# Optimization experiments

Hardware: AMD Instinct MI355X
Metric: run time of the kernel (lower is better)

Reference implementation:

```python
import math
import jax, jax.numpy as jnp
import numpy as np

B, N, D, H, NI, NL, NS, MID = 32, 2048, 256, 8, 64, 3, 32, 3


def _ln(x, g, b, eps=1e-5):
    m = jnp.mean(x, axis=-1, keepdims=True)
    v = jnp.mean((x - m) ** 2, axis=-1, keepdims=True)
    return (x - m) * jax.lax.rsqrt(v + eps) * g + b


def _mab(Q, K, mask, Wq, bq, Wk, bk, Wv, bv, Wo, bo, g0, b0, g1, b1):
    # torch's split(dim_split,2)+cat(...,0) == reshape to (B, n, H, dh)
    dh = D // H
    q = (Q @ Wq + bq).reshape(Q.shape[0], Q.shape[1], H, dh)
    k = (K @ Wk + bk).reshape(K.shape[0], K.shape[1], H, dh)
    v = (K @ Wv + bv).reshape(K.shape[0], K.shape[1], H, dh)
    A = jnp.einsum('bqhd,bkhd->bhqk', q, k) / math.sqrt(D)  # note: sqrt(dim_V), faithful
    A = jnp.where(mask[:, None, None, :] == 0, -1e4, A)
    A = jax.nn.softmax(A, axis=-1)
    o = q + jnp.einsum('bhqk,bkhd->bqhd', A, v)
    O = o.reshape(Q.shape[0], Q.shape[1], D)
    O = _ln(O, g0, b0)
    O = O + jax.nn.relu(O @ Wo + bo)
    return _ln(O, g1, b1)


def _forward(x_values, y_target, point_mask, proj_W, proj_b, isab_I,
             isab_Wq, isab_bq, isab_Wk, isab_bk, isab_Wv, isab_bv,
             isab_Wo, isab_bo, isab_g0, isab_b0, isab_g1, isab_b1,
             pma_S, pma_Wq, pma_bq, pma_Wk, pma_bk, pma_Wv, pma_bv,
             pma_Wo, pma_bo, pma_g0, pma_b0, pma_g1, pma_b1):
    # input_dim == max_input_dim, so the zero-padded feature build is a concat
    feats = jnp.concatenate([x_values, y_target[..., None]], axis=-1)  # (B, N, MID+1)
    x = jax.nn.gelu(feats @ proj_W + proj_b, approximate=False)
    ones_mask = jnp.ones((x.shape[0], NI), jnp.float32)
    stk = (isab_Wq, isab_bq, isab_Wk, isab_bk, isab_Wv, isab_bv,
           isab_Wo, isab_bo, isab_g0, isab_b0, isab_g1, isab_b1)
    for l in range(NL):
        I = jnp.broadcast_to(isab_I[l][None], (x.shape[0], NI, D))
        h = _mab(I, x, point_mask, *[a[l, 0] for a in stk])   # mab0: inducing pts attend to X
        x = _mab(x, h, ones_mask, *[a[l, 1] for a in stk])    # mab1: X attends to H (all valid)
    S = jnp.broadcast_to(pma_S[None], (x.shape[0], NS, D))
    return _mab(S, x, point_mask, pma_Wq, pma_bq, pma_Wk, pma_bk, pma_Wv,
                pma_bv, pma_Wo, pma_bo, pma_g0, pma_b0, pma_g1, pma_b1)


def setup_inputs():
    key = jax.random.key(0)
    ks = iter(jax.random.split(key, 40))
    def nrm(shape, s=0.05):
        return jax.random.normal(next(ks), shape, dtype=jnp.float32) * s
    z = lambda shape: jnp.zeros(shape, jnp.float32)
    o = lambda shape: jnp.ones(shape, jnp.float32)
    return {
        'x_values': jax.random.normal(next(ks), (B, N, MID), jnp.float32),
        'y_target': jax.random.normal(next(ks), (B, N), jnp.float32),
        'point_mask': jax.random.randint(next(ks), (B, N), 0, 2).astype(jnp.float32),
        'proj_W': nrm((MID + 1, D)), 'proj_b': z((D,)),
        'isab_I': nrm((NL, NI, D), 0.1),
        'isab_Wq': nrm((NL, 2, D, D)), 'isab_bq': z((NL, 2, D)),
        'isab_Wk': nrm((NL, 2, D, D)), 'isab_bk': z((NL, 2, D)),
        'isab_Wv': nrm((NL, 2, D, D)), 'isab_bv': z((NL, 2, D)),
        'isab_Wo': nrm((NL, 2, D, D)), 'isab_bo': z((NL, 2, D)),
        'isab_g0': o((NL, 2, D)), 'isab_b0': z((NL, 2, D)),
        'isab_g1': o((NL, 2, D)), 'isab_b1': z((NL, 2, D)),
        'pma_S': nrm((NS, D), 0.1),
        'pma_Wq': nrm((D, D)), 'pma_bq': z((D,)),
        'pma_Wk': nrm((D, D)), 'pma_bk': z((D,)),
        'pma_Wv': nrm((D, D)), 'pma_bv': z((D,)),
        'pma_Wo': nrm((D, D)), 'pma_bo': z((D,)),
        'pma_g0': o((D,)), 'pma_b0': z((D,)),
        'pma_g1': o((D,)), 'pma_b1': z((D,)),
    }


def reference(x_values, y_target, point_mask, proj_W, proj_b, isab_I,
              isab_Wq, isab_bq, isab_Wk, isab_bk, isab_Wv, isab_bv,
              isab_Wo, isab_bo, isab_g0, isab_b0, isab_g1, isab_b1,
              pma_S, pma_Wq, pma_bq, pma_Wk, pma_bk, pma_Wv, pma_bv,
              pma_Wo, pma_bo, pma_g0, pma_b0, pma_g1, pma_b1):
    return _forward(x_values, y_target, point_mask, proj_W, proj_b, isab_I,
                    isab_Wq, isab_bq, isab_Wk, isab_bk, isab_Wv, isab_bv,
                    isab_Wo, isab_bo, isab_g0, isab_b0, isab_g1, isab_b1,
                    pma_S, pma_Wq, pma_bq, pma_Wk, pma_bk, pma_Wv, pma_bv,
                    pma_Wo, pma_bo, pma_g0, pma_b0, pma_g1, pma_b1)
```

## Files before the change

### kernel.cpp

```cpp
#include <hip/hip_runtime.h>
#include <hip/hip_bf16.h>


typedef __attribute__((ext_vector_type(8))) short short8;
typedef __attribute__((ext_vector_type(4))) float f32x4;
typedef __attribute__((ext_vector_type(4))) ushort ushort4v;

__device__ __forceinline__ ushort f2bf(float f) {
  uint u = __builtin_bit_cast(uint, f);
  u += 0x7fffu + ((u >> 16) & 1u);
  return (ushort)(u >> 16);
}
__device__ __forceinline__ float bf2f(ushort h) {
  uint u = (uint)h << 16;
  return __builtin_bit_cast(float, u);
}

__global__ __launch_bounds__(256) void prep_weights(
    const float* __restrict__ Wq, const float* __restrict__ Wk,
    const float* __restrict__ Wv, const float* __restrict__ Wo,
    const float* __restrict__ pWq, const float* __restrict__ pWk,
    const float* __restrict__ pWv, const float* __restrict__ pWo,
    ushort* __restrict__ wt)
{
  __shared__ float tile[64][65];
  const int m = blockIdx.y;
  const int t = blockIdx.x;
  const int tr = (t >> 2) * 64;
  const int tc = (t & 3) * 64;
  const float* src;
  if (m < 24) {
    int l = m >> 3, s = (m >> 2) & 1, w = m & 3;
    const float* base = (w == 0) ? Wq : (w == 1) ? Wk : (w == 2) ? Wv : Wo;
    src = base + (size_t)(l * 2 + s) * 65536;
  } else {
    int w = m & 3;
    src = (w == 0) ? pWq : (w == 1) ? pWk : (w == 2) ? pWv : pWo;
  }
  const int tid = threadIdx.x;
  const int cn = tid & 63;
  const int rk = tid >> 6;
#pragma unroll
  for (int j = 0; j < 16; ++j) {
    int kl = rk + j * 4;
    tile[kl][cn] = src[(size_t)(tr + kl) * 256 + tc + cn];
  }
  __syncthreads();
  ushort* dst = wt + (size_t)m * 65536;
#pragma unroll
  for (int j = 0; j < 16; ++j) {
    int nl = rk + j * 4;
    dst[(size_t)(tc + nl) * 256 + tr + cn] = f2bf(tile[cn][nl]);
  }
}

__global__ __launch_bounds__(256) void proj_gelu(
    const float* __restrict__ xv, const float* __restrict__ yt,
    const float* __restrict__ pW, const float* __restrict__ pb,
    ushort* __restrict__ xb)
{
  const int d = threadIdx.x;
  const int row0 = blockIdx.x * 8;
  const float w0 = pW[d], w1 = pW[256 + d], w2 = pW[512 + d], w3 = pW[768 + d];
  const float bz = pb[d];
#pragma unroll
  for (int rr = 0; rr < 8; ++rr) {
    int row = row0 + rr;
    float f0 = xv[(size_t)row * 3 + 0];
    float f1 = xv[(size_t)row * 3 + 1];
    float f2 = xv[(size_t)row * 3 + 2];
    float f3 = yt[row];
    float a = bz + f0 * w0 + f1 * w1 + f2 * w2 + f3 * w3;
    float g = 0.5f * a * (1.f + erff(a * 0.70710678118654752f));
    xb[(size_t)row * 256 + d] = f2bf(g);
  }
}

__global__ __launch_bounds__(256) void gemm_q(
    const float* __restrict__ iI, const float* __restrict__ pS,
    const ushort* __restrict__ wt, const float* __restrict__ ibq,
    const float* __restrict__ pbq, ushort* __restrict__ q_all)
{
  const int bq = blockIdx.x;
  const float* A; const ushort* Wt; const float* bias; ushort* out; int M;
  if (bq < 3) { A = iI + bq * 16384; Wt = wt + (size_t)(bq * 8) * 65536; bias = ibq + bq * 512; out = q_all + bq * 16384; M = 64; }
  else        { A = pS; Wt = wt + (size_t)24 * 65536; bias = pbq; out = q_all + 49152; M = 32; }
  const int tid = threadIdx.x;
  const int wave = tid >> 6, lane = tid & 63;
  const int l15 = lane & 15, l4 = lane >> 4, koff = l4 * 8;
  f32x4 acc[4][4];
#pragma unroll
  for (int i = 0; i < 4; ++i)
#pragma unroll
    for (int j = 0; j < 4; ++j) acc[i][j] = (f32x4)0.f;
#pragma unroll
  for (int ks = 0; ks < 8; ++ks) {
    short8 af[4];
#pragma unroll
    for (int mf = 0; mf < 4; ++mf) {
      if (mf * 16 < M) {
        const float* ap = A + (size_t)(mf * 16 + l15) * 256 + ks * 32 + koff;
        float4 f0 = *(const float4*)ap;
        float4 f1 = *(const float4*)(ap + 4);
        short8 sv;
        sv[0] = (short)f2bf(f0.x); sv[1] = (short)f2bf(f0.y);
        sv[2] = (short)f2bf(f0.z); sv[3] = (short)f2bf(f0.w);
        sv[4] = (short)f2bf(f1.x); sv[5] = (short)f2bf(f1.y);
        sv[6] = (short)f2bf(f1.z); sv[7] = (short)f2bf(f1.w);
        af[mf] = sv;
      } else af[mf] = (short8)0;
    }
#pragma unroll
    for (int nf = 0; nf < 4; ++nf) {
      short8 bf = *(const short8*)(Wt + (size_t)(wave * 64 + nf * 16 + l15) * 256 + ks * 32 + koff);
#pragma unroll
      for (int mf = 0; mf < 4; ++mf)
        acc[mf][nf] = __builtin_amdgcn_mfma_f32_16x16x32_bf16(af[mf], bf, acc[mf][nf], 0, 0, 0);
    }
  }
#pragma unroll
  for (int mf = 0; mf < 4; ++mf) {
    if (mf * 16 >= M) continue;
#pragma unroll
    for (int nf = 0; nf < 4; ++nf) {
      int col = wave * 64 + nf * 16 + l15;
      float bcol = bias[col];
#pragma unroll
      for (int r = 0; r < 4; ++r)
        out[(size_t)(mf * 16 + l4 * 4 + r) * 256 + col] = f2bf(acc[mf][nf][r] + bcol);
    }
  }
}

template <int EPI, bool OUTF32, int COLS>
__global__ __launch_bounds__(COLS * 2, (COLS == 128) ? 3 : 2) void gemm_bp(
    const ushort* __restrict__ A,
    const ushort* __restrict__ Wt0, const ushort* __restrict__ Wt1, const ushort* __restrict__ Wt2,
    const float* __restrict__ b0, const float* __restrict__ b1, const float* __restrict__ b2,
    void* __restrict__ o0, void* __restrict__ o1, void* __restrict__ o2,
    const float* __restrict__ lng, const float* __restrict__ lnb)
{
  constexpr int WC = COLS / 64;
  constexpr int PS = COLS * 64;
  __shared__ __align__(16) char Bs[4 * PS];
  __shared__ float redbuf[(EPI == 3) ? 1280 : 4];
  const int y = blockIdx.z;
  const ushort* Wt = (y == 0) ? Wt0 : ((y == 1) ? Wt1 : Wt2);
  const float* bias = (y == 0) ? b0 : ((y == 1) ? b1 : b2);
  void* outp = (y == 0) ? o0 : ((y == 1) ? o1 : o2);
  const int pcol = blockIdx.y * COLS;

  const int tid = threadIdx.x;
  const int wave = tid >> 6, lane = tid & 63;
  const int wc = wave % WC, wr = wave / WC;
  const int l15 = lane & 15, l4 = lane >> 4;
  const int row0 = blockIdx.x * 128;
  const int sn = tid >> 1, sseg = tid & 1;

  f32x4 acc[4][4];
#pragma unroll
  for (int i = 0; i < 4; ++i)
#pragma unroll
    for (int j = 0; j < 4; ++j) acc[i][j] = (f32x4)0.f;

#pragma unroll
  for (int half = 0; half < 2; ++half) {
    if (half) __syncthreads();
    {
      const ushort* src = Wt + (size_t)(pcol + sn) * 256 + half * 128 + sseg * 64;
#pragma unroll
      for (int c = 0; c < 8; ++c) {
        uint4 w = *(const uint4*)(src + c * 8);
        int plane = sseg * 2 + (c >> 2);
        char* dst = Bs + plane * PS + sn * 64 + (((c & 3) * 16) ^ (((sn >> 1) & 3) << 4));
        *(uint4*)dst = w;
      }
    }
    __syncthreads();
#pragma unroll
    for (int ks = 0; ks < 4; ++ks) {
      short8 af[4];
#pragma unroll
      for (int mfa = 0; mfa < 4; ++mfa)
        af[mfa] = *(const short8*)(A + (size_t)(row0 + wr * 64 + mfa * 16 + l15) * 256 + half * 128 + ks * 32 + l4 * 8);
#pragma unroll
      for (int nfb = 0; nfb < 4; ++nfb) {
        int n = wc * 64 + nfb * 16 + l15;
        short8 bf = *(const short8*)(Bs + ks * PS + n * 64 + ((l4 * 16) ^ (((n >> 1) & 3) << 4)));
#pragma unroll
        for (int mfa = 0; mfa < 4; ++mfa)
          acc[mfa][nfb] = __builtin_amdgcn_mfma_f32_16x16x32_bf16(bf, af[mfa], acc[mfa][nfb], 0, 0, 0);
      }
    }
  }

  if constexpr (EPI == 0) {
#pragma unroll
    for (int nfb = 0; nfb < 4; ++nfb) {
      int col0 = pcol + wc * 64 + nfb * 16 + l4 * 4;
      f32x4 bv = *(const f32x4*)(bias + col0);
#pragma unroll
      for (int mfa = 0; mfa < 4; ++mfa) {
        size_t row = (size_t)row0 + wr * 64 + mfa * 16 + l15;
        ushort4v pk;
#pragma unroll
        for (int i = 0; i < 4; ++i) pk[i] = f2bf(acc[mfa][nfb][i] + bv[i]);
        *(ushort4v*)((ushort*)outp + row * 256 + col0) = pk;
      }
    }
  } else {
    float* red1 = redbuf;
    float* red2 = redbuf + 512;
    float* mv_ = redbuf + 1024;
    float* rv_ = redbuf + 1152;
    float s1[4] = {0.f, 0.f, 0.f, 0.f}, s2[4] = {0.f, 0.f, 0.f, 0.f};
#pragma unroll
    for (int nfb = 0; nfb < 4; ++nfb) {
      int col0 = wc * 64 + nfb * 16 + l4 * 4;
      f32x4 bv = *(const f32x4*)(bias + col0);
#pragma unroll
      for (int mfa = 0; mfa < 4; ++mfa) {
        size_t row = (size_t)row0 + wr * 64 + mfa * 16 + l15;
        ushort4v rz = *(const ushort4v*)(A + row * 256 + col0);
#pragma unroll
        for (int i = 0; i < 4; ++i) {
          float z = bf2f(rz[i]) + fmaxf(acc[mfa][nfb][i] + bv[i], 0.f);
          acc[mfa][nfb][i] = z;
          s1[mfa] += z;
          s2[mfa] += z * z;
        }
      }
    }
#pragma unroll
    for (int mfa = 0; mfa < 4; ++mfa) {
      s1[mfa] += __shfl_xor(s1[mfa], 16); s1[mfa] += __shfl_xor(s1[mfa], 32);
      s2[mfa] += __shfl_xor(s2[mfa], 16); s2[mfa] += __shfl_xor(s2[mfa], 32);
    }
    if (l4 == 0) {
#pragma unroll
      for (int mfa = 0; mfa < 4; ++mfa) {
        red1[wc * 128 + wr * 64 + mfa * 16 + l15] = s1[mfa];
        red2[wc * 128 + wr * 64 + mfa * 16 + l15] = s2[mfa];
      }
    }
    __syncthreads();
    if (tid < 128) {
      float m1 = red1[tid] + red1[128 + tid] + red1[256 + tid] + red1[384 + tid];
      float m2 = red2[tid] + red2[128 + tid] + red2[256 + tid] + red2[384 + tid];
      float mean = m1 * 0.00390625f;
      float var = m2 * 0.00390625f - mean * mean;
      mv_[tid] = mean;
      rv_[tid] = rsqrtf(var + 1e-5f);
    }
    __syncthreads();
#pragma unroll
    for (int nfb = 0; nfb < 4; ++nfb) {
      int col0 = wc * 64 + nfb * 16 + l4 * 4;
      f32x4 gg = *(const f32x4*)(lng + col0);
      f32x4 bb = *(const f32x4*)(lnb + col0);
#pragma unroll
      for (int mfa = 0; mfa < 4; ++mfa) {
        int lr = wr * 64 + mfa * 16 + l15;
        size_t row = (size_t)row0 + lr;
        float mean = mv_[lr], rs = rv_[lr];
        if constexpr (OUTF32) {
          f32x4 w;
#pragma unroll
          for (int i = 0; i < 4; ++i) w[i] = (acc[mfa][nfb][i] - mean) * rs * gg[i] + bb[i];
          *(f32x4*)((float*)outp + row * 256 + col0) = w;
        } else {
          ushort4v pk;
#pragma unroll
          for (int i = 0; i < 4; ++i) pk[i] = f2bf((acc[mfa][nfb][i] - mean) * rs * gg[i] + bb[i]);
          *(ushort4v*)((ushort*)outp + row * 256 + col0) = pk;
        }
      }
    }
  }
}

template <int MF>
__global__ __launch_bounds__(512) void attn_big(
    const ushort* __restrict__ qb, const ushort* __restrict__ kb,
    const ushort* __restrict__ vb, const float* __restrict__ mask,
    ushort* __restrict__ O)
{
  __shared__ __align__(16) ushort Ps[8][64][72];
  __shared__ __align__(16) ushort Vt[8][32][72];
  const int h = blockIdx.x, b = blockIdx.y;
  const int tid = threadIdx.x;
  const int w = tid >> 6, lane = tid & 63;
  const int l15 = lane & 15, l4 = lane >> 4;
  const int koff = l4 * 8;
  const int kvbase = b * 2048;

  short8 qf[MF];
#pragma unroll
  for (int mf = 0; mf < MF; ++mf)
    qf[mf] = *(const short8*)(qb + (size_t)(mf * 16 + l15) * 256 + h * 32 + koff);

  f32x4 Oa[MF][2];
  float Mr[MF][4], Lr[MF][4];
#pragma unroll
  for (int mf = 0; mf < MF; ++mf) {
    Oa[mf][0] = (f32x4)0.f; Oa[mf][1] = (f32x4)0.f;
#pragma unroll
    for (int r = 0; r < 4; ++r) { Mr[mf][r] = -1e30f; Lr[mf][r] = 0.f; }
  }

  for (int c = 0; c < 4; ++c) {
    const int kc = w * 256 + c * 64;
    f32x4 S[MF][4];
#pragma unroll
    for (int nf = 0; nf < 4; ++nf) {
      short8 kf = *(const short8*)(kb + (size_t)(kvbase + kc + nf * 16 + l15) * 256 + h * 32 + koff);
#pragma unroll
      for (int mf = 0; mf < MF; ++mf)
        S[mf][nf] = __builtin_amdgcn_mfma_f32_16x16x32_bf16(qf[mf], kf, (f32x4)0.f, 0, 0, 0);
    }
    float mv[4];
#pragma unroll
    for (int nf = 0; nf < 4; ++nf)
      mv[nf] = mask[(size_t)b * 2048 + kc + nf * 16 + l15];
#pragma unroll
    for (int mf = 0; mf < MF; ++mf)
#pragma unroll
      for (int nf = 0; nf < 4; ++nf)
#pragma unroll
        for (int r = 0; r < 4; ++r) {
          float s = S[mf][nf][r] * 0.0625f;
          S[mf][nf][r] = (mv[nf] != 0.f) ? s : -1e4f;
        }
#pragma unroll
    for (int mf = 0; mf < MF; ++mf)
#pragma unroll
      for (int r = 0; r < 4; ++r) {
        float pm = fmaxf(fmaxf(S[mf][0][r], S[mf][1][r]), fmaxf(S[mf][2][r], S[mf][3][r]));
        pm = fmaxf(pm, __shfl_xor(pm, 1));
        pm = fmaxf(pm, __shfl_xor(pm, 2));
        pm = fmaxf(pm, __shfl_xor(pm, 4));
        pm = fmaxf(pm, __shfl_xor(pm, 8));
        float Mnew = fmaxf(Mr[mf][r], pm);
        float corr = __expf(Mr[mf][r] - Mnew);
        Mr[mf][r] = Mnew;
        float rs = 0.f;
#pragma unroll
        for (int nf = 0; nf < 4; ++nf) {
          float p = __expf(S[mf][nf][r] - Mnew);
          S[mf][nf][r] = p;
          rs += p;
        }
        rs += __shfl_xor(rs, 1);
        rs += __shfl_xor(rs, 2);
        rs += __shfl_xor(rs, 4);
        rs += __shfl_xor(rs, 8);
        Lr[mf][r] = Lr[mf][r] * corr + rs;
        Oa[mf][0][r] *= corr;
        Oa[mf][1][r] *= corr;
      }
#pragma unroll
    for (int dblk = 0; dblk < 4; ++dblk) {
      short8 vv = *(const short8*)(vb + (size_t)(kvbase + kc + lane) * 256 + h * 32 + dblk * 8);
#pragma unroll
      for (int j = 0; j < 8; ++j) Vt[w][dblk * 8 + j][lane] = (ushort)vv[j];
    }
#pragma unroll
    for (int mf = 0; mf < MF; ++mf)
#pragma unroll
      for (int nf = 0; nf < 4; ++nf)
#pragma unroll
        for (int r = 0; r < 4; ++r)
          Ps[w][mf * 16 + l4 * 4 + r][nf * 16 + l15] = f2bf(S[mf][nf][r]);
#pragma unroll
    for (int ks = 0; ks < 2; ++ks) {
      short8 pf[MF];
#pragma unroll
      for (int mf = 0; mf < MF; ++mf)
        pf[mf] = *(const short8*)&Ps[w][mf * 16 + l15][ks * 32 + koff];
#pragma unroll
      for (int nf2 = 0; nf2 < 2; ++nf2) {
        short8 vf = *(const short8*)&Vt[w][nf2 * 16 + l15][ks * 32 + koff];
#pragma unroll
        for (int mf = 0; mf < MF; ++mf)
          Oa[mf][nf2] = __builtin_amdgcn_mfma_f32_16x16x32_bf16(pf[mf], vf, Oa[mf][nf2], 0, 0, 0);
      }
    }
  }

  __syncthreads();
  float* Mw = (float*)&Ps[0][0][0];
  float* Lw = Mw + 512;
  float* Ow = Lw + 512;
#pragma unroll
  for (int mf = 0; mf < MF; ++mf)
#pragma unroll
    for (int r = 0; r < 4; ++r) {
      int row = mf * 16 + l4 * 4 + r;
      if (l15 == 0) { Mw[w * 64 + row] = Mr[mf][r]; Lw[w * 64 + row] = Lr[mf][r]; }
#pragma unroll
      for (int nf2 = 0; nf2 < 2; ++nf2)
        Ow[(w * 64 + row) * 33 + nf2 * 16 + l15] = Oa[mf][nf2][r];
    }
  __syncthreads();
  const int NQ = MF * 16;
  int row = tid >> 3, dg = tid & 7;
  if (row < NQ) {
    float mm = -1e30f;
#pragma unroll
    for (int s = 0; s < 8; ++s) mm = fmaxf(mm, Mw[s * 64 + row]);
    float den = 0.f, es[8];
#pragma unroll
    for (int s = 0; s < 8; ++s) {
      es[s] = __expf(Mw[s * 64 + row] - mm);
      den += Lw[s * 64 + row] * es[s];
    }
    float invden = 1.f / den;
    ushort4v pk;
#pragma unroll
    for (int i = 0; i < 4; ++i) {
      int d = dg * 4 + i;
      float num = 0.f;
#pragma unroll
      for (int s = 0; s < 8; ++s) num += Ow[(s * 64 + row) * 33 + d] * es[s];
      float qv = bf2f(qb[(size_t)row * 256 + h * 32 + d]);
      pk[i] = f2bf(qv + num * invden);
    }
    *(ushort4v*)(O + (size_t)(b * NQ + row) * 256 + h * 32 + dg * 4) = pk;
  }
}

__global__ __launch_bounds__(512) void attn_small(
    const ushort* __restrict__ qb, const ushort* __restrict__ kb,
    const ushort* __restrict__ vb, const float* __restrict__ lng,
    const float* __restrict__ lnb, ushort* __restrict__ O)
{
  __shared__ __align__(16) ushort Ps[8][64][72];
  __shared__ __align__(16) ushort Vt[8][32][72];
  __shared__ float red1[8][64], red2[8][64], mv_[64], rv_[64];
  const int qt = blockIdx.x, b = blockIdx.y;
  const int tid = threadIdx.x;
  const int w = tid >> 6, lane = tid & 63;
  const int l15 = lane & 15, l4 = lane >> 4;
  const int koff = l4 * 8;
  const size_t qrow0 = (size_t)b * 2048 + qt * 64;
  const int kvbase = b * 64;
  const int h = w;

  short8 qf[4];
#pragma unroll
  for (int mf = 0; mf < 4; ++mf)
    qf[mf] = *(const short8*)(qb + (qrow0 + mf * 16 + l15) * 256 + h * 32 + koff);

  f32x4 S[4][4];
#pragma unroll
  for (int nf = 0; nf < 4; ++nf) {
    short8 kf = *(const short8*)(kb + (size_t)(kvbase + nf * 16 + l15) * 256 + h * 32 + koff);
#pragma unroll
    for (int mf = 0; mf < 4; ++mf)
      S[mf][nf] = __builtin_amdgcn_mfma_f32_16x16x32_bf16(qf[mf], kf, (f32x4)0.f, 0, 0, 0);
  }
  float Lr[4][4];
#pragma unroll
  for (int mf = 0; mf < 4; ++mf)
#pragma unroll
    for (int r = 0; r < 4; ++r) {
      float pm = fmaxf(fmaxf(S[mf][0][r], S[mf][1][r]), fmaxf(S[mf][2][r], S[mf][3][r])) * 0.0625f;
      pm = fmaxf(pm, __shfl_xor(pm, 1));
      pm = fmaxf(pm, __shfl_xor(pm, 2));
      pm = fmaxf(pm, __shfl_xor(pm, 4));
      pm = fmaxf(pm, __shfl_xor(pm, 8));
      float rs = 0.f;
#pragma unroll
      for (int nf = 0; nf < 4; ++nf) {
        float p = __expf(S[mf][nf][r] * 0.0625f - pm);
        S[mf][nf][r] = p;
        rs += p;
      }
      rs += __shfl_xor(rs, 1);
      rs += __shfl_xor(rs, 2);
      rs += __shfl_xor(rs, 4);
      rs += __shfl_xor(rs, 8);
      Lr[mf][r] = rs;
    }
#pragma unroll
  for (int dblk = 0; dblk < 4; ++dblk) {
    short8 vv = *(const short8*)(vb + (size_t)(kvbase + lane) * 256 + h * 32 + dblk * 8);
#pragma unroll
    for (int j = 0; j < 8; ++j) Vt[w][dblk * 8 + j][lane] = (ushort)vv[j];
  }
#pragma unroll
  for (int mf = 0; mf < 4; ++mf)
#pragma unroll
    for (int nf = 0; nf < 4; ++nf)
#pragma unroll
      for (int r = 0; r < 4; ++r)
        Ps[w][mf * 16 + l4 * 4 + r][nf * 16 + l15] = f2bf(S[mf][nf][r]);
  f32x4 Oa[4][2];
#pragma unroll
  for (int mf = 0; mf < 4; ++mf) { Oa[mf][0] = (f32x4)0.f; Oa[mf][1] = (f32x4)0.f; }
#pragma unroll
  for (int ks = 0; ks < 2; ++ks) {
    short8 pf[4];
#pragma unroll
    for (int mf = 0; mf < 4; ++mf)
      pf[mf] = *(const short8*)&Ps[w][mf * 16 + l15][ks * 32 + koff];
#pragma unroll
    for (int nf2 = 0; nf2 < 2; ++nf2) {
      short8 vf = *(const short8*)&Vt[w][nf2 * 16 + l15][ks * 32 + koff];
#pragma unroll
      for (int mf = 0; mf < 4; ++mf)
        Oa[mf][nf2] = __builtin_amdgcn_mfma_f32_16x16x32_bf16(pf[mf], vf, Oa[mf][nf2], 0, 0, 0);
    }
  }
  float s1[4][4], s2[4][4];
#pragma unroll
  for (int mf = 0; mf < 4; ++mf)
#pragma unroll
    for (int r = 0; r < 4; ++r) {
      float invL = 1.f / Lr[mf][r];
      s1[mf][r] = 0.f; s2[mf][r] = 0.f;
#pragma unroll
      for (int nf2 = 0; nf2 < 2; ++nf2) {
        int col = h * 32 + nf2 * 16 + l15;
        size_t row = qrow0 + mf * 16 + l4 * 4 + r;
        float z = bf2f(qb[row * 256 + col]) + Oa[mf][nf2][r] * invL;
        Oa[mf][nf2][r] = z;
        s1[mf][r] += z;
        s2[mf][r] += z * z;
      }
#pragma unroll
      for (int off = 1; off < 16; off <<= 1) {
        s1[mf][r] += __shfl_xor(s1[mf][r], off);
        s2[mf][r] += __shfl_xor(s2[mf][r], off);
      }
      if (l15 == 0) {
        int row = mf * 16 + l4 * 4 + r;
        red1[w][row] = s1[mf][r];
        red2[w][row] = s2[mf][r];
      }
    }
  __syncthreads();
  if (tid < 64) {
    float m1 = 0.f, m2 = 0.f;
#pragma unroll
    for (int s = 0; s < 8; ++s) { m1 += red1[s][tid]; m2 += red2[s][tid]; }
    float mean = m1 * 0.00390625f;
    float var = m2 * 0.00390625f - mean * mean;
    mv_[tid] = mean;
    rv_[tid] = rsqrtf(var + 1e-5f);
  }
  __syncthreads();
#pragma unroll
  for (int nf2 = 0; nf2 < 2; ++nf2) {
    int col = h * 32 + nf2 * 16 + l15;
    float gc = lng[col], bc = lnb[col];
#pragma unroll
    for (int mf = 0; mf < 4; ++mf)
#pragma unroll
      for (int r = 0; r < 4; ++r) {
        int row = mf * 16 + l4 * 4 + r;
        float v = (Oa[mf][nf2][r] - mv_[row]) * rv_[row] * gc + bc;
        O[(qrow0 + row) * 256 + col] = f2bf(v);
      }
  }
}

__global__ __launch_bounds__(256) void ln4(
    const ushort* __restrict__ in, ushort* __restrict__ out,
    const float* __restrict__ g, const float* __restrict__ bb)
{
  const int w = threadIdx.x >> 6, lane = threadIdx.x & 63;
  const size_t row = (size_t)blockIdx.x * 4 + w;
  ushort4v u = *(const ushort4v*)(in + row * 256 + lane * 4);
  float v[4];
#pragma unroll
  for (int i = 0; i < 4; ++i) v[i] = bf2f(u[i]);
  float s1 = v[0] + v[1] + v[2] + v[3];
  float s2 = v[0] * v[0] + v[1] * v[1] + v[2] * v[2] + v[3] * v[3];
#pragma unroll
  for (int off = 1; off < 64; off <<= 1) {
    s1 += __shfl_xor(s1, off);
    s2 += __shfl_xor(s2, off);
  }
  float mean = s1 * 0.00390625f;
  float var = s2 * 0.00390625f - mean * mean;
  float rs = rsqrtf(var + 1e-5f);
  f32x4 gg = *(const f32x4*)(g + lane * 4);
  f32x4 bv = *(const f32x4*)(bb + lane * 4);
  ushort4v p;
#pragma unroll
  for (int i = 0; i < 4; ++i) p[i] = f2bf((v[i] - mean) * rs * gg[i] + bv[i]);
  *(ushort4v*)(out + row * 256 + lane * 4) = p;
}

extern "C" void kernel_launch(void* const* d_in, const int* in_sizes, int n_in,
                              void* d_out, int out_size, void* d_ws, size_t ws_size,
                              hipStream_t stream) {
  const float* xv = (const float*)d_in[0];
  const float* yt = (const float*)d_in[1];
  const float* pmask = (const float*)d_in[2];
  const float* prW = (const float*)d_in[3];
  const float* prb = (const float*)d_in[4];
  const float* iI = (const float*)d_in[5];
  const float* iWq = (const float*)d_in[6];
  const float* ibq = (const float*)d_in[7];
  const float* iWk = (const float*)d_in[8];
  const float* ibk = (const float*)d_in[9];
  const float* iWv = (const float*)d_in[10];
  const float* ibv = (const float*)d_in[11];
  const float* iWo = (const float*)d_in[12];
  const float* ibo = (const float*)d_in[13];
  const float* ig0 = (const float*)d_in[14];
  const float* ib0 = (const float*)d_in[15];
  const float* ig1 = (const float*)d_in[16];
  const float* ib1 = (const float*)d_in[17];
  const float* pS = (const float*)d_in[18];
  const float* pWq = (const float*)d_in[19];
  const float* pbq = (const float*)d_in[20];
  const float* pWk = (const float*)d_in[21];
  const float* pbk = (const float*)d_in[22];
  const float* pWv = (const float*)d_in[23];
  const float* pbv = (const float*)d_in[24];
  const float* pWo = (const float*)d_in[25];
  const float* pbo = (const float*)d_in[26];
  const float* pg0 = (const float*)d_in[27];
  const float* pb0 = (const float*)d_in[28];
  const float* pg1 = (const float*)d_in[29];
  const float* pb1 = (const float*)d_in[30];

  char* ws = (char*)d_ws;
  if (ws_size < 172621824u) return;
  ushort* xb = (ushort*)(ws + 0);
  ushort* ob = (ushort*)(ws + 33554432);
  ushort* hb = (ushort*)(ws + 67108864);
  ushort* qbw = (ushort*)(ws + 68157440);
  ushort* kbw = (ushort*)(ws + 101711872);
  ushort* vbw = (ushort*)(ws + 135266304);
  ushort* wt = (ushort*)(ws + 168820736);
  ushort* q_all = (ushort*)(ws + 172490752);

  prep_weights<<<dim3(16, 28), 256, 0, stream>>>(iWq, iWk, iWv, iWo, pWq, pWk, pWv, pWo, wt);
  proj_gelu<<<8192, 256, 0, stream>>>(xv, yt, prW, prb, xb);
  gemm_q<<<4, 256, 0, stream>>>(iI, pS, wt, ibq, pbq, q_all);

  for (int l = 0; l < 3; ++l) {
    const int s0 = l * 2, s1 = l * 2 + 1;
    const ushort* wk = wt + (size_t)(l * 8 + 1) * 65536;
    const ushort* wv = wt + (size_t)(l * 8 + 2) * 65536;
    const ushort* wo0 = wt + (size_t)(l * 8 + 3) * 65536;
    const ushort* wq1 = wt + (size_t)(l * 8 + 4) * 65536;
    const ushort* wk1 = wt + (size_t)(l * 8 + 5) * 65536;
    const ushort* wv1 = wt + (size_t)(l * 8 + 6) * 65536;
    const ushort* wo1 = wt + (size_t)(l * 8 + 7) * 65536;
    gemm_bp<0, false, 128><<<dim3(512, 2, 3), 256, 0, stream>>>(
        xb, wk, wv, wq1, ibk + s0 * 256, ibv + s0 * 256, ibq + s1 * 256,
        kbw, vbw, qbw, nullptr, nullptr);
    attn_big<4><<<dim3(8, 32), 512, 0, stream>>>(q_all + l * 16384, kbw, vbw, pmask, ob);
    ln4<<<512, 256, 0, stream>>>(ob, ob, ig0 + s0 * 256, ib0 + s0 * 256);
    gemm_bp<3, false, 256><<<dim3(16, 1, 1), 512, 0, stream>>>(
        ob, wo0, wo0, wo0, ibo + s0 * 256, ibo + s0 * 256, ibo + s0 * 256,
        hb, hb, hb, ig1 + s0 * 256, ib1 + s0 * 256);
    gemm_bp<0, false, 128><<<dim3(16, 2, 2), 256, 0, stream>>>(
        hb, wk1, wv1, wv1, ibk + s1 * 256, ibv + s1 * 256, ibv + s1 * 256,
        kbw, vbw, vbw, nullptr, nullptr);
    attn_small<<<dim3(32, 32), 512, 0, stream>>>(qbw, kbw, vbw, ig0 + s1 * 256, ib0 + s1 * 256, ob);
    gemm_bp<3, false, 256><<<dim3(512, 1, 1), 512, 0, stream>>>(
        ob, wo1, wo1, wo1, ibo + s1 * 256, ibo + s1 * 256, ibo + s1 * 256,
        xb, xb, xb, ig1 + s1 * 256, ib1 + s1 * 256);
  }
  gemm_bp<0, false, 128><<<dim3(512, 2, 2), 256, 0, stream>>>(
      xb, wt + (size_t)25 * 65536, wt + (size_t)26 * 65536, wt + (size_t)26 * 65536,
      pbk, pbv, pbv, kbw, vbw, vbw, nullptr, nullptr);
  attn_big<2><<<dim3(8, 32), 512, 0, stream>>>(q_all + 49152, kbw, vbw, pmask, ob);
  ln4<<<256, 256, 0, stream>>>(ob, ob, pg0, pb0);
  gemm_bp<3, true, 256><<<dim3(8, 1, 1), 512, 0, stream>>>(
      ob, wt + (size_t)27 * 65536, wt + (size_t)27 * 65536, wt + (size_t)27 * 65536,
      pbo, pbo, pbo, d_out, d_out, d_out, pg1, pb1);
}
```

Baseline: 915.4 us.

## Stage GEMM epilogue through LDS for coalesced stores and linearize block order

The GEMM epilogues now write bf16 results into the swizzled shared-memory buffer and then copy them to global memory with 16-byte, row-contiguous stores, replacing scattered 8-byte stores. The 3D grid becomes a 1D grid whose index is decoded so that all column-tiles and weight matrices for one row block run next to each other, which should improve L2 reuse of the A rows. The occupancy hint for the 128-column variant is raised from 3 to 4 blocks per CU. These changes add extra barriers and LDS traffic, and the higher occupancy target may force register spills.

```diff
diff --git a/kernel.cpp b/kernel.cpp
--- a/kernel.cpp
+++ b/kernel.cpp
@@ -133,28 +133,34 @@
 }
 
 template <int EPI, bool OUTF32, int COLS>
-__global__ __launch_bounds__(COLS * 2, (COLS == 128) ? 3 : 2) void gemm_bp(
+__global__ __launch_bounds__(COLS * 2, (COLS == 128) ? 4 : 2) void gemm_bp(
     const ushort* __restrict__ A,
     const ushort* __restrict__ Wt0, const ushort* __restrict__ Wt1, const ushort* __restrict__ Wt2,
     const float* __restrict__ b0, const float* __restrict__ b1, const float* __restrict__ b2,
     void* __restrict__ o0, void* __restrict__ o1, void* __restrict__ o2,
-    const float* __restrict__ lng, const float* __restrict__ lnb)
+    const float* __restrict__ lng, const float* __restrict__ lnb,
+    int ny, int nyz)
 {
   constexpr int WC = COLS / 64;
   constexpr int PS = COLS * 64;
+  constexpr int ROWB = COLS * 2;
   __shared__ __align__(16) char Bs[4 * PS];
   __shared__ float redbuf[(EPI == 3) ? 1280 : 4];
-  const int y = blockIdx.z;
-  const ushort* Wt = (y == 0) ? Wt0 : ((y == 1) ? Wt1 : Wt2);
-  const float* bias = (y == 0) ? b0 : ((y == 1) ? b1 : b2);
-  void* outp = (y == 0) ? o0 : ((y == 1) ? o1 : o2);
-  const int pcol = blockIdx.y * COLS;
+  const int bid = blockIdx.x;
+  const int bx = bid / nyz;
+  const int brem = bid % nyz;
+  const int y = brem % ny;
+  const int z = brem / ny;
+  const ushort* Wt = (z == 0) ? Wt0 : ((z == 1) ? Wt1 : Wt2);
+  const float* bias = (z == 0) ? b0 : ((z == 1) ? b1 : b2);
+  void* outp = (z == 0) ? o0 : ((z == 1) ? o1 : o2);
+  const int pcol = y * COLS;
 
   const int tid = threadIdx.x;
   const int wave = tid >> 6, lane = tid & 63;
   const int wc = wave % WC, wr = wave / WC;
   const int l15 = lane & 15, l4 = lane >> 4;
-  const int row0 = blockIdx.x * 128;
+  const int row0 = bx * 128;
   const int sn = tid >> 1, sseg = tid & 1;
 
   f32x4 acc[4][4];
@@ -195,17 +201,32 @@
   }
 
   if constexpr (EPI == 0) {
+    __syncthreads();
 #pragma unroll
     for (int nfb = 0; nfb < 4; ++nfb) {
-      int col0 = pcol + wc * 64 + nfb * 16 + l4 * 4;
-      f32x4 bv = *(const f32x4*)(bias + col0);
+      f32x4 bv = *(const f32x4*)(bias + pcol + wc * 64 + nfb * 16 + l4 * 4);
+      int colb = wc * 128 + nfb * 32 + l4 * 8;
 #pragma unroll
       for (int mfa = 0; mfa < 4; ++mfa) {
-        size_t row = (size_t)row0 + wr * 64 + mfa * 16 + l15;
+        int row = wr * 64 + mfa * 16 + l15;
         ushort4v pk;
 #pragma unroll
         for (int i = 0; i < 4; ++i) pk[i] = f2bf(acc[mfa][nfb][i] + bv[i]);
-        *(ushort4v*)((ushort*)outp + row * 256 + col0) = pk;
+        *(ushort4v*)(Bs + row * ROWB + (colb ^ ((row & 7) << 4))) = pk;
+      }
+    }
+    __syncthreads();
+    const int srow = tid >> 2, seg = tid & 3;
+#pragma unroll
+    for (int rr = 0; rr < 2; ++rr) {
+      int row = srow + rr * 64;
+      int x = (row & 7) << 4;
+      ushort* gdst = (ushort*)outp + (size_t)(row0 + row) * 256 + pcol;
+#pragma unroll
+      for (int it = 0; it < 4; ++it) {
+        int colb = seg * 16 + it * 64;
+        uint4 v = *(const uint4*)(Bs + row * ROWB + (colb ^ x));
+        *(uint4*)(gdst + colb / 2) = v;
       }
     }
   } else {
@@ -224,10 +245,10 @@
         ushort4v rz = *(const ushort4v*)(A + row * 256 + col0);
 #pragma unroll
         for (int i = 0; i < 4; ++i) {
-          float z = bf2f(rz[i]) + fmaxf(acc[mfa][nfb][i] + bv[i], 0.f);
-          acc[mfa][nfb][i] = z;
-          s1[mfa] += z;
-          s2[mfa] += z * z;
+          float zz = bf2f(rz[i]) + fmaxf(acc[mfa][nfb][i] + bv[i], 0.f);
+          acc[mfa][nfb][i] = zz;
+          s1[mfa] += zz;
+          s2[mfa] += zz * zz;
         }
       }
     }
@@ -258,22 +279,34 @@
       int col0 = wc * 64 + nfb * 16 + l4 * 4;
       f32x4 gg = *(const f32x4*)(lng + col0);
       f32x4 bb = *(const f32x4*)(lnb + col0);
+      int colb = col0 * 2;
 #pragma unroll
       for (int mfa = 0; mfa < 4; ++mfa) {
         int lr = wr * 64 + mfa * 16 + l15;
-        size_t row = (size_t)row0 + lr;
         float mean = mv_[lr], rs = rv_[lr];
         if constexpr (OUTF32) {
           f32x4 w;
 #pragma unroll
           for (int i = 0; i < 4; ++i) w[i] = (acc[mfa][nfb][i] - mean) * rs * gg[i] + bb[i];
-          *(f32x4*)((float*)outp + row * 256 + col0) = w;
+          *(f32x4*)((float*)outp + ((size_t)row0 + lr) * 256 + col0) = w;
         } else {
           ushort4v pk;
 #pragma unroll
           for (int i = 0; i < 4; ++i) pk[i] = f2bf((acc[mfa][nfb][i] - mean) * rs * gg[i] + bb[i]);
-          *(ushort4v*)((ushort*)outp + row * 256 + col0) = pk;
+          *(ushort4v*)(Bs + lr * ROWB + (colb ^ ((lr & 7) << 4))) = pk;
         }
+      }
+    }
+    if constexpr (!OUTF32) {
+      __syncthreads();
+      const int srow = tid >> 2, seg = tid & 3;
+      int x = (srow & 7) << 4;
+      ushort* gdst = (ushort*)outp + (size_t)(row0 + srow) * 256;
+#pragma unroll
+      for (int it = 0; it < 8; ++it) {
+        int colb = seg * 16 + it * 64;
+        uint4 v = *(const uint4*)(Bs + srow * ROWB + (colb ^ x));
+        *(uint4*)(gdst + colb / 2) = v;
       }
     }
   }
@@ -652,28 +685,28 @@
     const ushort* wk1 = wt + (size_t)(l * 8 + 5) * 65536;
     const ushort* wv1 = wt + (size_t)(l * 8 + 6) * 65536;
     const ushort* wo1 = wt + (size_t)(l * 8 + 7) * 65536;
-    gemm_bp<0, false, 128><<<dim3(512, 2, 3), 256, 0, stream>>>(
+    gemm_bp<0, false, 128><<<3072, 256, 0, stream>>>(
         xb, wk, wv, wq1, ibk + s0 * 256, ibv + s0 * 256, ibq + s1 * 256,
-        kbw, vbw, qbw, nullptr, nullptr);
+        kbw, vbw, qbw, nullptr, nullptr, 2, 6);
     attn_big<4><<<dim3(8, 32), 512, 0, stream>>>(q_all + l * 16384, kbw, vbw, pmask, ob);
     ln4<<<512, 256, 0, stream>>>(ob, ob, ig0 + s0 * 256, ib0 + s0 * 256);
-    gemm_bp<3, false, 256><<<dim3(16, 1, 1), 512, 0, stream>>>(
+    gemm_bp<3, false, 256><<<16, 512, 0, stream>>>(
         ob, wo0, wo0, wo0, ibo + s0 * 256, ibo + s0 * 256, ibo + s0 * 256,
-        hb, hb, hb, ig1 + s0 * 256, ib1 + s0 * 256);
-    gemm_bp<0, false, 128><<<dim3(16, 2, 2), 256, 0, stream>>>(
+        hb, hb, hb, ig1 + s0 * 256, ib1 + s0 * 256, 1, 1);
+    gemm_bp<0, false, 128><<<64, 256, 0, stream>>>(
         hb, wk1, wv1, wv1, ibk + s1 * 256, ibv + s1 * 256, ibv + s1 * 256,
-        kbw, vbw, vbw, nullptr, nullptr);
+        kbw, vbw, vbw, nullptr, nullptr, 2, 4);
     attn_small<<<dim3(32, 32), 512, 0, stream>>>(qbw, kbw, vbw, ig0 + s1 * 256, ib0 + s1 * 256, ob);
-    gemm_bp<3, false, 256><<<dim3(512, 1, 1), 512, 0, stream>>>(
+    gemm_bp<3, false, 256><<<512, 512, 0, stream>>>(
         ob, wo1, wo1, wo1, ibo + s1 * 256, ibo + s1 * 256, ibo + s1 * 256,
-        xb, xb, xb, ig1 + s1 * 256, ib1 + s1 * 256);
-  }
-  gemm_bp<0, false, 128><<<dim3(512, 2, 2), 256, 0, stream>>>(
+        xb, xb, xb, ig1 + s1 * 256, ib1 + s1 * 256, 1, 1);
+  }
+  gemm_bp<0, false, 128><<<2048, 256, 0, stream>>>(
       xb, wt + (size_t)25 * 65536, wt + (size_t)26 * 65536, wt + (size_t)26 * 65536,
-      pbk, pbv, pbv, kbw, vbw, vbw, nullptr, nullptr);
+      pbk, pbv, pbv, kbw, vbw, vbw, nullptr, nullptr, 2, 4);
   attn_big<2><<<dim3(8, 32), 512, 0, stream>>>(q_all + 49152, kbw, vbw, pmask, ob);
   ln4<<<256, 256, 0, stream>>>(ob, ob, pg0, pb0);
-  gemm_bp<3, true, 256><<<dim3(8, 1, 1), 512, 0, stream>>>(
+  gemm_bp<3, true, 256><<<8, 512, 0, stream>>>(
       ob, wt + (size_t)27 * 65536, wt + (size_t)27 * 65536, wt + (size_t)27 * 65536,
-      pbo, pbo, pbo, d_out, d_out, d_out, pg1, pb1);
-}
+      pbo, pbo, pbo, d_out, d_out, d_out, pg1, pb1, 1, 1);
+}
```

Result: faster. 872.4 us (-4.7%).
